# Kernel tuning notes

Hardware: AMD Instinct MI355X
Metric: run time of the kernel (lower is better)

The kernel has to match this reference:

```python
import jax, jax.numpy as jnp
import numpy as np

N = 50000      # neurons
R = 10         # max receptors per neuron
D = 5          # max delay (steps)
E = 10000000   # recurrent synapses
B = 1          # batch
DT = 1.0
LR_SCALE = 1.0
REC_DAMP = 0.4       # recurrent_dampening_factor
DAMPENING = 0.3      # dampening_factor (surrogate grad)


def setup_inputs() -> dict:
    key = jax.random.key(0)
    ks = jax.random.split(key, 20)
    inputs = jax.random.normal(ks[0], (B, R * N), jnp.float32) * 0.01
    z_buf = (jax.random.uniform(ks[1], (B, D * N)) < 0.02).astype(jnp.float32)
    v = jax.random.uniform(ks[2], (B, N), jnp.float32)
    r = jnp.zeros((B, N), jnp.float32)
    asc_1 = jax.random.normal(ks[3], (B, N), jnp.float32) * 0.01
    asc_2 = jax.random.normal(ks[4], (B, N), jnp.float32) * 0.01
    psc_rise = jax.random.uniform(ks[5], (B, R * N), jnp.float32) * 0.01
    psc = jax.random.uniform(ks[6], (B, R * N), jnp.float32) * 0.01
    rec_w = jax.random.normal(ks[7], (E,), jnp.float32) * 0.01
    rows = jax.random.randint(ks[8], (E,), 0, R * N, jnp.int32)
    cols = jax.random.randint(ks[9], (E,), 0, D * N, jnp.int32)
    rec_idx = jnp.stack([rows, cols], axis=1)
    # voltages are normalized by (V_th - E_L): v_th -> 1, e_l -> 0, v_reset -> 0
    v_th = jnp.ones((N,), jnp.float32)
    e_l = jnp.zeros((N,), jnp.float32)
    v_reset = jnp.zeros((N,), jnp.float32)
    g = jax.random.uniform(ks[10], (N,), jnp.float32, 3.0, 6.0)
    tau_m = jax.random.uniform(ks[11], (N,), jnp.float32, 5.0, 30.0)
    decay = jnp.exp(-DT / tau_m)
    current_factor = jax.random.uniform(ks[12], (N,), jnp.float32, 0.5, 1.5)
    t_ref = jnp.full((N,), 2.2, jnp.float32)
    k = jax.random.normal(ks[13], (N, 2), jnp.float32)  # stored in inv-sigmoid domain
    asc_amps = jax.random.normal(ks[14], (N, 2), jnp.float32) * 0.1
    tau_syn = jax.random.uniform(ks[15], (R * N,), jnp.float32, 2.0, 10.0)
    syn_decay = jnp.exp(-DT / tau_syn)
    psc_initial = jnp.asarray(np.e, jnp.float32) / tau_syn
    voltage_scale = jnp.full((N,), 30.0, jnp.float32)
    voltage_offset = jnp.full((N,), -70.0, jnp.float32)
    return dict(inputs=inputs, z_buf=z_buf, v=v, r=r, asc_1=asc_1, asc_2=asc_2,
                psc_rise=psc_rise, psc=psc, rec_w=rec_w, rec_idx=rec_idx,
                v_th=v_th, e_l=e_l, v_reset=v_reset, g=g, decay=decay,
                current_factor=current_factor, t_ref=t_ref, k=k, asc_amps=asc_amps,
                syn_decay=syn_decay, psc_initial=psc_initial,
                voltage_scale=voltage_scale, voltage_offset=voltage_offset)


def reference(inputs, z_buf, v, r, asc_1, asc_2, psc_rise, psc, rec_w, rec_idx,
              v_th, e_l, v_reset, g, decay, current_factor, t_ref, k, asc_amps,
              syn_decay, psc_initial, voltage_scale, voltage_offset):
    # one BillehColumn time step
    shaped = z_buf.reshape(B, D, N)          # (B, max_delay, N)
    prev_z = shaped[:, 0]
    # gradient-dampened spike buffer (fwd value identical to z_buf)
    dampened = z_buf * REC_DAMP
    rec_z = jax.lax.stop_gradient(z_buf - dampened) + dampened
    # sparse synaptic matmul: rows = neuron*R + receptor, cols = delay-slot neuron
    vals = rec_w[:, None] * rec_z.T[rec_idx[:, 1]]                       # (E, B)
    i_rec = jax.ops.segment_sum(vals, rec_idx[:, 0], num_segments=R * N).T  # (B, R*N)
    rec_inputs = i_rec * LR_SCALE + inputs
    # double-exponential synapse dynamics
    new_psc_rise = syn_decay * psc_rise + rec_inputs * psc_initial
    new_psc = psc * syn_decay + DT * syn_decay * psc_rise
    # refractory counter
    new_r = jnp.maximum(r + prev_z * t_ref - DT, 0.0)
    # after-spike currents (k stored in inv-sigmoid domain)
    kk = jax.nn.sigmoid(k)
    new_asc_1 = jnp.exp(-DT * kk[:, 0]) * asc_1 + prev_z * asc_amps[:, 0]
    new_asc_2 = jnp.exp(-DT * kk[:, 1]) * asc_2 + prev_z * asc_amps[:, 1]
    # membrane update: sum psc over receptors
    input_current = psc.reshape(B, N, R).sum(-1)
    new_v = decay * v + current_factor * (input_current + asc_1 + asc_2 + g * e_l)
    # surrogate-spike threshold (forward: heaviside)
    v_sc = (new_v - v_th) / (v_th - e_l)
    new_z = (v_sc > 0.0).astype(jnp.float32)
    new_z = jnp.where(new_r > 0.0, 0.0, new_z)
    # hard reset
    new_v = jnp.where(new_z > 0.5, jnp.broadcast_to(v_reset, new_v.shape), new_v)
    # shift delay buffer
    new_z_buf = jnp.concatenate([new_z[:, None], shaped[:, :-1]], axis=1).reshape(B, D * N)
    out_v = new_v * voltage_scale + voltage_offset
    return (new_z, out_v, new_z_buf, new_v, new_r, new_asc_1, new_asc_2,
            new_psc_rise, new_psc)
```

## Files before the change

### kernel.cpp

```cpp
#include <hip/hip_runtime.h>

namespace {

constexpr int N  = 50000;
constexpr int R  = 10;
constexpr int DD = 5;
constexpr int RN = R * N;
constexpr int DN = DD * N;
constexpr int E  = 10000000;
constexpr int EP = E / 2;

constexpr int ZB_BLOCKS = (DN + 255) / 256;
constexpr int ZB_WORDS  = ZB_BLOCKS * 256 / 32;

constexpr int AC_BLOCKS   = (RN / 4 + 255) / 256;
constexpr int NEUR_BLOCKS = (N + 255) / 256;
constexpr int SH_BLOCKS   = ((DN - N) / 4 + 255) / 256;
constexpr int PRE_BLOCKS  = ZB_BLOCKS + AC_BLOCKS + NEUR_BLOCKS + SH_BLOCKS;

__global__ __launch_bounds__(256) void pre_kernel(
    const float*  __restrict__ z_buf,
    unsigned int* __restrict__ bits,
    const float4* __restrict__ inputs,
    float4*       __restrict__ acc,
    const float*  __restrict__ v,
    const float*  __restrict__ r,
    const float*  __restrict__ asc1,
    const float*  __restrict__ asc2,
    const float*  __restrict__ psc,
    const float*  __restrict__ v_th,
    const float*  __restrict__ e_l,
    const float*  __restrict__ v_reset,
    const float*  __restrict__ g,
    const float*  __restrict__ decay,
    const float*  __restrict__ current_factor,
    const float*  __restrict__ t_ref,
    const float2* __restrict__ k,
    const float2* __restrict__ asc_amps,
    const float*  __restrict__ voltage_scale,
    const float*  __restrict__ voltage_offset,
    float*        __restrict__ out)
{
    int b = blockIdx.x;
    int tid = threadIdx.x;

    if (b < ZB_BLOCKS) {
        int i = b * 256 + tid;
        float zv = (i < DN) ? z_buf[i] : 0.0f;
        unsigned long long m = __ballot(zv != 0.0f);
        if ((tid & 63) == 0) {
            int w = i >> 5;
            bits[w]     = (unsigned int)m;
            bits[w + 1] = (unsigned int)(m >> 32);
        }
        return;
    }
    b -= ZB_BLOCKS;
    if (b < AC_BLOCKS) {
        int i = b * 256 + tid;
        if (i < RN / 4) acc[i] = inputs[i];
        return;
    }
    b -= AC_BLOCKS;
    if (b < NEUR_BLOCKS) {
        int n = b * 256 + tid;
        if (n >= N) return;

        float prev_z = z_buf[n];

        const float2* p2 = reinterpret_cast<const float2*>(psc + n * R);
        float ic = 0.0f;
#pragma unroll
        for (int t = 0; t < R / 2; ++t) {
            float2 p = p2[t];
            ic += p.x + p.y;
        }

        float new_r = fmaxf(r[n] + prev_z * t_ref[n] - 1.0f, 0.0f);

        float2 kk = k[n];
        float2 aa = asc_amps[n];
        float s0 = 1.0f / (1.0f + expf(-kk.x));
        float s1 = 1.0f / (1.0f + expf(-kk.y));
        float a1_old = asc1[n];
        float a2_old = asc2[n];
        float new_a1 = expf(-s0) * a1_old + prev_z * aa.x;
        float new_a2 = expf(-s1) * a2_old + prev_z * aa.y;

        float el = e_l[n];
        float new_v = decay[n] * v[n]
                    + current_factor[n] * (ic + a1_old + a2_old + g[n] * el);

        float vth = v_th[n];
        float v_sc = (new_v - vth) / (vth - el);
        float nz = (v_sc > 0.0f) ? 1.0f : 0.0f;
        if (new_r > 0.0f) nz = 0.0f;
        if (nz > 0.5f) new_v = v_reset[n];

        out[0 * N + n]  = nz;
        out[1 * N + n]  = new_v * voltage_scale[n] + voltage_offset[n];
        out[2 * N + n]  = nz;
        out[7 * N + n]  = new_v;
        out[8 * N + n]  = new_r;
        out[9 * N + n]  = new_a1;
        out[10 * N + n] = new_a2;
        return;
    }
    b -= NEUR_BLOCKS;
    {
        int i = b * 256 + tid;
        if (i < (DN - N) / 4) {
            const float4* src = reinterpret_cast<const float4*>(z_buf);
            float4* dst = reinterpret_cast<float4*>(out + 3 * N);
            dst[i] = src[i];
        }
        return;
    }
}

__global__ __launch_bounds__(256) void scatter_kernel(
    const float* __restrict__ rec_w,
    const int4*  __restrict__ idx4,
    const unsigned int* __restrict__ bits_g,
    float*       __restrict__ acc)
{
    __shared__ unsigned int bits[ZB_WORDS];
    for (int i = threadIdx.x; i < ZB_WORDS; i += 256)
        bits[i] = bits_g[i];
    __syncthreads();

    int stride = gridDim.x * 256;
    int p = blockIdx.x * 256 + threadIdx.x;
    for (; p + stride < EP; p += 2 * stride) {
        int4 a = idx4[p];
        int4 c = idx4[p + stride];
        unsigned int wa0 = bits[a.y >> 5];
        unsigned int wa1 = bits[a.w >> 5];
        unsigned int wc0 = bits[c.y >> 5];
        unsigned int wc1 = bits[c.w >> 5];
        if ((wa0 >> (a.y & 31)) & 1u) atomicAdd(acc + a.x, rec_w[2 * p]);
        if ((wa1 >> (a.w & 31)) & 1u) atomicAdd(acc + a.z, rec_w[2 * p + 1]);
        if ((wc0 >> (c.y & 31)) & 1u) atomicAdd(acc + c.x, rec_w[2 * (p + stride)]);
        if ((wc1 >> (c.w & 31)) & 1u) atomicAdd(acc + c.z, rec_w[2 * (p + stride) + 1]);
    }
    if (p < EP) {
        int4 a = idx4[p];
        unsigned int wa0 = bits[a.y >> 5];
        unsigned int wa1 = bits[a.w >> 5];
        if ((wa0 >> (a.y & 31)) & 1u) atomicAdd(acc + a.x, rec_w[2 * p]);
        if ((wa1 >> (a.w & 31)) & 1u) atomicAdd(acc + a.z, rec_w[2 * p + 1]);
    }
}

__global__ __launch_bounds__(256) void syn_kernel(
    const float4* __restrict__ acc,
    const float4* __restrict__ psc_rise,
    const float4* __restrict__ psc,
    const float4* __restrict__ syn_decay,
    const float4* __restrict__ psc_initial,
    float4* __restrict__ out_psc_rise,
    float4* __restrict__ out_psc,
    int n4)
{
    int j = blockIdx.x * 256 + threadIdx.x;
    if (j >= n4) return;
    float4 sd = syn_decay[j];
    float4 pr = psc_rise[j];
    float4 pi = psc_initial[j];
    float4 ac = acc[j];
    float4 ps = psc[j];
    float4 opr, ops;
    opr.x = sd.x * pr.x + ac.x * pi.x;
    opr.y = sd.y * pr.y + ac.y * pi.y;
    opr.z = sd.z * pr.z + ac.z * pi.z;
    opr.w = sd.w * pr.w + ac.w * pi.w;
    ops.x = ps.x * sd.x + sd.x * pr.x;
    ops.y = ps.y * sd.y + sd.y * pr.y;
    ops.z = ps.z * sd.z + sd.z * pr.z;
    ops.w = ps.w * sd.w + sd.w * pr.w;
    out_psc_rise[j] = opr;
    out_psc[j]      = ops;
}

}

extern "C" void kernel_launch(void* const* d_in, const int* in_sizes, int n_in,
                              void* d_out, int out_size, void* d_ws, size_t ws_size,
                              hipStream_t stream) {
    const float* inputs         = (const float*)d_in[0];
    const float* z_buf          = (const float*)d_in[1];
    const float* v              = (const float*)d_in[2];
    const float* r              = (const float*)d_in[3];
    const float* asc1           = (const float*)d_in[4];
    const float* asc2           = (const float*)d_in[5];
    const float* psc_rise       = (const float*)d_in[6];
    const float* psc            = (const float*)d_in[7];
    const float* rec_w          = (const float*)d_in[8];
    const int*   rec_idx        = (const int*)d_in[9];
    const float* v_th           = (const float*)d_in[10];
    const float* e_l            = (const float*)d_in[11];
    const float* v_reset        = (const float*)d_in[12];
    const float* g              = (const float*)d_in[13];
    const float* decay          = (const float*)d_in[14];
    const float* current_factor = (const float*)d_in[15];
    const float* t_ref          = (const float*)d_in[16];
    const float* k              = (const float*)d_in[17];
    const float* asc_amps       = (const float*)d_in[18];
    const float* syn_decay      = (const float*)d_in[19];
    const float* psc_initial    = (const float*)d_in[20];
    const float* voltage_scale  = (const float*)d_in[21];
    const float* voltage_offset = (const float*)d_in[22];

    float* out = (float*)d_out;
    float* acc = (float*)d_ws;
    unsigned int* bits = (unsigned int*)(acc + RN);

    pre_kernel<<<PRE_BLOCKS, 256, 0, stream>>>(
        z_buf, bits, (const float4*)inputs, (float4*)acc,
        v, r, asc1, asc2, psc, v_th, e_l, v_reset, g, decay,
        current_factor, t_ref, (const float2*)k, (const float2*)asc_amps,
        voltage_scale, voltage_offset, out);

    scatter_kernel<<<1280, 256, 0, stream>>>(
        rec_w, (const int4*)rec_idx, bits, acc);

    syn_kernel<<<(RN / 4 + 255) / 256, 256, 0, stream>>>(
        (const float4*)acc, (const float4*)psc_rise, (const float4*)psc,
        (const float4*)syn_decay, (const float4*)psc_initial,
        (float4*)(out + 11 * N), (float4*)(out + 21 * N), RN / 4);
}
```

Measured before the change: 35.08 us.

## Software-pipeline scatter loads over two edge halves and move delay-buffer shift into scatter

The scatter kernel now walks two halves of the edge list at once and prefetches the next index pair before doing the current atomics, so load latency overlaps with the atomic work. It also uses 512-thread blocks on a 1024-block grid and copies the spike bitmask into shared memory with 16-byte loads. The delay-buffer shift copy moves out of the pre kernel and into the tail of the scatter kernel. This cuts the pre kernel's block count and hides the copy behind scatter work, at the cost of more registers per thread and a less regular access stride.

```diff
diff --git a/kernel.cpp b/kernel.cpp
--- a/kernel.cpp
+++ b/kernel.cpp
@@ -9,14 +9,19 @@
 constexpr int DN = DD * N;
 constexpr int E  = 10000000;
 constexpr int EP = E / 2;
+constexpr int EPH = EP / 2;
 
 constexpr int ZB_BLOCKS = (DN + 255) / 256;
 constexpr int ZB_WORDS  = ZB_BLOCKS * 256 / 32;
 
 constexpr int AC_BLOCKS   = (RN / 4 + 255) / 256;
 constexpr int NEUR_BLOCKS = (N + 255) / 256;
-constexpr int SH_BLOCKS   = ((DN - N) / 4 + 255) / 256;
-constexpr int PRE_BLOCKS  = ZB_BLOCKS + AC_BLOCKS + NEUR_BLOCKS + SH_BLOCKS;
+constexpr int PRE_BLOCKS  = ZB_BLOCKS + AC_BLOCKS + NEUR_BLOCKS;
+
+constexpr int SC_BLOCK = 512;
+constexpr int SC_GRID  = 1024;
+
+constexpr int SYN_BLOCKS = (RN / 4 + 255) / 256;
 
 __global__ __launch_bounds__(256) void pre_kernel(
     const float*  __restrict__ z_buf,
@@ -62,7 +67,7 @@
         return;
     }
     b -= AC_BLOCKS;
-    if (b < NEUR_BLOCKS) {
+    {
         int n = b * 256 + tid;
         if (n >= N) return;
 
@@ -72,8 +77,8 @@
         float ic = 0.0f;
 #pragma unroll
         for (int t = 0; t < R / 2; ++t) {
-            float2 p = p2[t];
-            ic += p.x + p.y;
+            float2 pp = p2[t];
+            ic += pp.x + pp.y;
         }
 
         float new_r = fmaxf(r[n] + prev_z * t_ref[n] - 1.0f, 0.0f);
@@ -104,51 +109,63 @@
         out[8 * N + n]  = new_r;
         out[9 * N + n]  = new_a1;
         out[10 * N + n] = new_a2;
-        return;
-    }
-    b -= NEUR_BLOCKS;
-    {
-        int i = b * 256 + tid;
-        if (i < (DN - N) / 4) {
-            const float4* src = reinterpret_cast<const float4*>(z_buf);
-            float4* dst = reinterpret_cast<float4*>(out + 3 * N);
-            dst[i] = src[i];
-        }
-        return;
-    }
-}
-
-__global__ __launch_bounds__(256) void scatter_kernel(
+    }
+}
+
+__device__ __forceinline__ void edge_pair(
+    const int4 a, int p, const unsigned int* bits,
+    const float* __restrict__ rec_w, float* __restrict__ acc)
+{
+    unsigned int w0 = bits[a.y >> 5];
+    unsigned int w1 = bits[a.w >> 5];
+    if ((w0 >> (a.y & 31)) & 1u) atomicAdd(acc + a.x, rec_w[2 * p]);
+    if ((w1 >> (a.w & 31)) & 1u) atomicAdd(acc + a.z, rec_w[2 * p + 1]);
+}
+
+__global__ __launch_bounds__(SC_BLOCK) void scatter_kernel(
     const float* __restrict__ rec_w,
     const int4*  __restrict__ idx4,
     const unsigned int* __restrict__ bits_g,
-    float*       __restrict__ acc)
+    float*       __restrict__ acc,
+    const float* __restrict__ z_buf,
+    float*       __restrict__ out)
 {
     __shared__ unsigned int bits[ZB_WORDS];
-    for (int i = threadIdx.x; i < ZB_WORDS; i += 256)
-        bits[i] = bits_g[i];
+    {
+        const uint4* src = reinterpret_cast<const uint4*>(bits_g);
+        uint4* dst = reinterpret_cast<uint4*>(bits);
+        for (int i = threadIdx.x; i < ZB_WORDS / 4; i += SC_BLOCK)
+            dst[i] = src[i];
+    }
     __syncthreads();
 
-    int stride = gridDim.x * 256;
-    int p = blockIdx.x * 256 + threadIdx.x;
-    for (; p + stride < EP; p += 2 * stride) {
-        int4 a = idx4[p];
-        int4 c = idx4[p + stride];
-        unsigned int wa0 = bits[a.y >> 5];
-        unsigned int wa1 = bits[a.w >> 5];
-        unsigned int wc0 = bits[c.y >> 5];
-        unsigned int wc1 = bits[c.w >> 5];
-        if ((wa0 >> (a.y & 31)) & 1u) atomicAdd(acc + a.x, rec_w[2 * p]);
-        if ((wa1 >> (a.w & 31)) & 1u) atomicAdd(acc + a.z, rec_w[2 * p + 1]);
-        if ((wc0 >> (c.y & 31)) & 1u) atomicAdd(acc + c.x, rec_w[2 * (p + stride)]);
-        if ((wc1 >> (c.w & 31)) & 1u) atomicAdd(acc + c.z, rec_w[2 * (p + stride) + 1]);
-    }
-    if (p < EP) {
-        int4 a = idx4[p];
-        unsigned int wa0 = bits[a.y >> 5];
-        unsigned int wa1 = bits[a.w >> 5];
-        if ((wa0 >> (a.y & 31)) & 1u) atomicAdd(acc + a.x, rec_w[2 * p]);
-        if ((wa1 >> (a.w & 31)) & 1u) atomicAdd(acc + a.z, rec_w[2 * p + 1]);
+    const int gs  = SC_GRID * SC_BLOCK;
+    const int gid = blockIdx.x * SC_BLOCK + threadIdx.x;
+
+    int pA = gid, pB = gid + EPH;
+    bool hA = pA < EPH;
+    bool hB = pB < EP;
+    int4 a = {0, 0, 0, 0}, b = {0, 0, 0, 0};
+    if (hA) a = idx4[pA];
+    if (hB) b = idx4[pB];
+    while (hA || hB) {
+        int nA = pA + gs, nB = pB + gs;
+        bool hnA = hA && (nA < EPH);
+        bool hnB = hB && (nB < EP);
+        int4 na = {0, 0, 0, 0}, nb = {0, 0, 0, 0};
+        if (hnA) na = idx4[nA];
+        if (hnB) nb = idx4[nB];
+        if (hA) edge_pair(a, pA, bits, rec_w, acc);
+        if (hB) edge_pair(b, pB, bits, rec_w, acc);
+        a = na; pA = nA; hA = hnA;
+        b = nb; pB = nB; hB = hnB;
+    }
+
+    {
+        const float4* src = reinterpret_cast<const float4*>(z_buf);
+        float4* dst = reinterpret_cast<float4*>(out + 3 * N);
+        for (int i = gid; i < (DN - N) / 4; i += gs)
+            dst[i] = src[i];
     }
 }
 
@@ -221,10 +238,10 @@
         current_factor, t_ref, (const float2*)k, (const float2*)asc_amps,
         voltage_scale, voltage_offset, out);
 
-    scatter_kernel<<<1280, 256, 0, stream>>>(
-        rec_w, (const int4*)rec_idx, bits, acc);
-
-    syn_kernel<<<(RN / 4 + 255) / 256, 256, 0, stream>>>(
+    scatter_kernel<<<SC_GRID, SC_BLOCK, 0, stream>>>(
+        rec_w, (const int4*)rec_idx, bits, acc, z_buf, out);
+
+    syn_kernel<<<SYN_BLOCKS, 256, 0, stream>>>(
         (const float4*)acc, (const float4*)psc_rise, (const float4*)psc,
         (const float4*)syn_decay, (const float4*)psc_initial,
         (float4*)(out + 11 * N), (float4*)(out + 21 * N), RN / 4);
```

After: 34.88 us. No clear change (-0.6%).
